# Kernel optimization log

Measured on AMD Instinct MI355X. Metric: run time of the kernel, lower is better.

The kernel has to match this reference:

```python
import jax, jax.numpy as jnp
import numpy as np

D_MODEL = 1024
NUM_HEADS = 16
MAX_LEN = 500
D_K = D_MODEL // NUM_HEADS


def setup_inputs() -> dict:
    key = jax.random.key(0)
    ks = jax.random.split(key, 10)
    B, L = 8, 500
    s = 1.0 / np.sqrt(D_MODEL)
    return {
        "query": jax.random.normal(ks[0], (B, L, D_MODEL), dtype=jnp.float32),
        "key": jax.random.normal(ks[1], (B, L, D_MODEL), dtype=jnp.float32),
        "value": jax.random.normal(ks[2], (B, L, D_MODEL), dtype=jnp.float32),
        "Wq": jax.random.normal(ks[3], (D_MODEL, D_MODEL), dtype=jnp.float32) * s,
        "bq": jnp.zeros((D_MODEL,), dtype=jnp.float32),
        "Wk": jax.random.normal(ks[4], (D_MODEL, D_MODEL), dtype=jnp.float32) * s,
        "bk": jnp.zeros((D_MODEL,), dtype=jnp.float32),
        "Wv": jax.random.normal(ks[5], (D_MODEL, D_MODEL), dtype=jnp.float32) * s,
        "bv": jnp.zeros((D_MODEL,), dtype=jnp.float32),
        "rel_emb": jax.random.normal(ks[6], (NUM_HEADS, 2 * MAX_LEN - 1), dtype=jnp.float32),
    }


def reference(query, key, value, Wq, bq, Wk, bk, Wv, bv, rel_emb):
    B, Lq, _ = query.shape
    Lk = key.shape[1]
    H, dk = NUM_HEADS, D_K
    # QKV projections -> [B, H, L, d]
    q = (query @ Wq + bq).reshape(B, Lq, H, dk).transpose(0, 2, 1, 3)
    k = (key @ Wk + bk).reshape(B, Lk, H, dk).transpose(0, 2, 1, 3)
    v = (value @ Wv + bv).reshape(B, Lk, H, dk).transpose(0, 2, 1, 3)
    scores = jnp.einsum('bhqd,bhkd->bhqk', q, k) / jnp.sqrt(jnp.float32(dk))
    # gathered relative-position bias: [H, Lq, Lk]
    rel_idx = jnp.arange(Lq)[:, None] - jnp.arange(Lk)[None, :] + MAX_LEN - 1
    bias = rel_emb[:, rel_idx]  # [H, Lq, Lk]
    scores = scores + bias[None]
    attn = jax.nn.softmax(scores, axis=-1)
    out = jnp.einsum('bhqk,bhkd->bhqd', attn, v)
    return out.transpose(0, 2, 1, 3).reshape(B, Lq, H * dk)
```

## Files before the change

### kernel.cpp

```cpp
#include <hip/hip_runtime.h>

typedef short bf16x8 __attribute__((ext_vector_type(8)));
typedef float f32x4 __attribute__((ext_vector_type(4)));
typedef unsigned uint4v __attribute__((ext_vector_type(4)));

#define B_    8
#define L_    500
#define LP    512
#define H_    16
#define DK    64
#define DM    1024
#define MP    4096
#define NT    8

static __device__ __forceinline__ unsigned short f2bf(float x) {
  unsigned u = __float_as_uint(x);
  u += 0x7fffu + ((u >> 16) & 1u);
  return (unsigned short)(u >> 16);
}

static __device__ __forceinline__ unsigned cvtpk(float lo, float hi) {
  unsigned r;
  asm("v_cvt_pk_bf16_f32 %0, %1, %2" : "=v"(r) : "v"(lo), "v"(hi));
  return r;
}

static __device__ __forceinline__ void gload16(const void* g, void* l) {
  __builtin_amdgcn_global_load_lds(
      (const __attribute__((address_space(1))) void*)g,
      (__attribute__((address_space(3))) void*)l, 16, 0, 0);
}

__global__ __launch_bounds__(256) void conv_x_kernel(
    const float* __restrict__ iq, const float* __restrict__ ik,
    const float* __restrict__ iv, unsigned short* __restrict__ X) {
  const int z = blockIdx.y;
  const float* src = (z == 0) ? iq : (z == 1) ? ik : iv;
  const size_t flat = (size_t)blockIdx.x * 256 + threadIdx.x;
  const size_t off = flat * 8;
  const int m = (int)(off >> 10);
  unsigned short o[8];
  if (m < 4000) {
    const float4 a = *(const float4*)(src + off);
    const float4 b = *(const float4*)(src + off + 4);
    o[0]=f2bf(a.x); o[1]=f2bf(a.y); o[2]=f2bf(a.z); o[3]=f2bf(a.w);
    o[4]=f2bf(b.x); o[5]=f2bf(b.y); o[6]=f2bf(b.z); o[7]=f2bf(b.w);
  } else {
#pragma unroll
    for (int i = 0; i < 8; ++i) o[i] = 0;
  }
  uint4 pk;
  pk.x = (unsigned)o[0] | ((unsigned)o[1] << 16);
  pk.y = (unsigned)o[2] | ((unsigned)o[3] << 16);
  pk.z = (unsigned)o[4] | ((unsigned)o[5] << 16);
  pk.w = (unsigned)o[6] | ((unsigned)o[7] << 16);
  *(uint4*)(X + (size_t)z * MP * DM + off) = pk;
}

__global__ __launch_bounds__(256) void conv_w_kernel(
    const float* __restrict__ wq, const float* __restrict__ wk,
    const float* __restrict__ wv, unsigned short* __restrict__ Wt) {
  const int z = blockIdx.y;
  const float* W = (z == 0) ? wq : (z == 1) ? wk : wv;
  const int k0 = (blockIdx.x >> 4) * 64;
  const int n0 = (blockIdx.x & 15) * 64;
  __shared__ float t[64][65];
  const int tid = threadIdx.x;
  const int row = tid >> 2;
  const int cb  = (tid & 3) * 16;
#pragma unroll
  for (int s = 0; s < 4; ++s) {
    const float4 v = *(const float4*)(W + (size_t)(k0 + row) * DM + n0 + cb + s * 4);
    t[row][cb + s * 4 + 0] = v.x; t[row][cb + s * 4 + 1] = v.y;
    t[row][cb + s * 4 + 2] = v.z; t[row][cb + s * 4 + 3] = v.w;
  }
  __syncthreads();
  const int nr = tid >> 2;
  const int kb = (tid & 3) * 16;
#pragma unroll
  for (int s = 0; s < 2; ++s) {
    unsigned short o[8];
#pragma unroll
    for (int e = 0; e < 8; ++e) o[e] = f2bf(t[kb + s * 8 + e][nr]);
    uint4 pk;
    pk.x = (unsigned)o[0] | ((unsigned)o[1] << 16);
    pk.y = (unsigned)o[2] | ((unsigned)o[3] << 16);
    pk.z = (unsigned)o[4] | ((unsigned)o[5] << 16);
    pk.w = (unsigned)o[6] | ((unsigned)o[7] << 16);
    *(uint4*)(Wt + (size_t)z * DM * DM + (size_t)(n0 + nr) * DM + k0 + kb + s * 8) = pk;
  }
}

__global__ __launch_bounds__(256) void gemm_qkv_kernel(
    const unsigned short* __restrict__ X, const unsigned short* __restrict__ Wt,
    const float* __restrict__ bq, const float* __restrict__ bk,
    const float* __restrict__ bv,
    unsigned short* __restrict__ qo, unsigned short* __restrict__ ko,
    unsigned short* __restrict__ vo) {
  const int z = blockIdx.y;
  const unsigned short* A  = X  + (size_t)z * MP * DM;
  const unsigned short* Bw = Wt + (size_t)z * DM * DM;
  const float* bias = (z == 0) ? bq : (z == 1) ? bk : bv;
  unsigned short* out = (z == 0) ? qo : (z == 1) ? ko : vo;

  const int bid = blockIdx.x;
  const int xg = bid & 7, y = bid >> 3;
  const int tm = xg + 8 * (y >> 3);
  const int tn = y & 7;
  const int tid = threadIdx.x;
  const int lane = tid & 63, wid = tid >> 6;
  const int wr = wid >> 1, wc = wid & 1;
  const int lg = lane >> 4, lr = lane & 15;

  __shared__ unsigned short sA[2][128 * 32];
  __shared__ unsigned short sB[2][128 * 32];

  const int c0 = tid, c1 = tid + 256;
  const int ar0 = c0 >> 2, ak0 = (c0 & 3) * 8;
  const int ar1 = c1 >> 2, ak1 = (c1 & 3) * 8;
  const unsigned short* Ab = A  + (size_t)tm * 128 * DM;
  const unsigned short* Bb = Bw + (size_t)tn * 128 * DM;

  f32x4 acc[4][4];
#pragma unroll
  for (int i = 0; i < 4; ++i)
#pragma unroll
    for (int j = 0; j < 4; ++j) acc[i][j] = (f32x4){0.f, 0.f, 0.f, 0.f};

  gload16(Ab + (size_t)ar0 * DM + ak0, &sA[0][c0 * 8]);
  gload16(Ab + (size_t)ar1 * DM + ak1, &sA[0][c1 * 8]);
  gload16(Bb + (size_t)ar0 * DM + ak0, &sB[0][c0 * 8]);
  gload16(Bb + (size_t)ar1 * DM + ak1, &sB[0][c1 * 8]);
  asm volatile("s_waitcnt vmcnt(0)" ::: "memory");
  __syncthreads();

  int cur = 0;
  for (int t = 0; t < 32; ++t) {
    if (t < 31) {
      const int kn = (t + 1) * 32;
      gload16(Ab + (size_t)ar0 * DM + kn + ak0, &sA[cur ^ 1][c0 * 8]);
      gload16(Ab + (size_t)ar1 * DM + kn + ak1, &sA[cur ^ 1][c1 * 8]);
      gload16(Bb + (size_t)ar0 * DM + kn + ak0, &sB[cur ^ 1][c0 * 8]);
      gload16(Bb + (size_t)ar1 * DM + kn + ak1, &sB[cur ^ 1][c1 * 8]);
    }
    bf16x8 af[4], bfr[4];
#pragma unroll
    for (int s = 0; s < 4; ++s) {
      af[s]  = *(const bf16x8*)&sA[cur][(wr * 64 + s * 16 + lr) * 32 + lg * 8];
      bfr[s] = *(const bf16x8*)&sB[cur][(wc * 64 + s * 16 + lr) * 32 + lg * 8];
    }
#pragma unroll
    for (int i = 0; i < 4; ++i)
#pragma unroll
      for (int j = 0; j < 4; ++j)
        acc[i][j] = __builtin_amdgcn_mfma_f32_16x16x32_bf16(af[i], bfr[j], acc[i][j], 0, 0, 0);
    asm volatile("s_waitcnt vmcnt(0)" ::: "memory");
    __syncthreads();
    cur ^= 1;
  }

  const int nbase = tn * 128 + wc * 64 + lr;
  float bias4[4];
#pragma unroll
  for (int ns = 0; ns < 4; ++ns) bias4[ns] = bias[nbase + ns * 16];

#pragma unroll
  for (int ms = 0; ms < 4; ++ms) {
#pragma unroll
    for (int r = 0; r < 4; ++r) {
      const int m = tm * 128 + wr * 64 + ms * 16 + lg * 4 + r;
      if (m < 4000) {
        const unsigned batch = (unsigned)m / 500u;
        const int lrow = m - (int)batch * 500;
#pragma unroll
        for (int ns = 0; ns < 4; ++ns) {
          const int n = nbase + ns * 16;
          const int hh = n >> 6, d = n & 63;
          out[(((size_t)batch * H_ + hh) * LP + lrow) * DK + d] =
              f2bf(acc[ms][ns][r] + bias4[ns]);
        }
      }
    }
  }
}

__global__ __launch_bounds__(256) void transpose_v_kernel(
    const unsigned short* __restrict__ v, unsigned short* __restrict__ vt) {
  const int bh = blockIdx.y;
  const int l0 = blockIdx.x * 64;
  __shared__ unsigned short t[64][72];
  const int tid = threadIdx.x;
  const int lrw = tid >> 2, dc = (tid & 3) * 16;
  const int gl = l0 + lrw;
  if (gl < L_) {
    *(uint4*)&t[lrw][dc]     = *(const uint4*)(v + ((size_t)bh * LP + gl) * DK + dc);
    *(uint4*)&t[lrw][dc + 8] = *(const uint4*)(v + ((size_t)bh * LP + gl) * DK + dc + 8);
  } else {
    const uint4 zz = {0u, 0u, 0u, 0u};
    *(uint4*)&t[lrw][dc]     = zz;
    *(uint4*)&t[lrw][dc + 8] = zz;
  }
  __syncthreads();
  const int dr = tid >> 2, lcb = (tid & 3) * 16;
#pragma unroll
  for (int s = 0; s < 2; ++s) {
    unsigned short e[8];
#pragma unroll
    for (int i = 0; i < 8; ++i) e[i] = t[lcb + s * 8 + i][dr];
    uint4 o;
    o.x = (unsigned)e[0] | ((unsigned)e[1] << 16);
    o.y = (unsigned)e[2] | ((unsigned)e[3] << 16);
    o.z = (unsigned)e[4] | ((unsigned)e[5] << 16);
    o.w = (unsigned)e[6] | ((unsigned)e[7] << 16);
    *(uint4*)(vt + ((size_t)bh * DK + dr) * LP + l0 + lcb + s * 8) = o;
  }
}

__global__ __launch_bounds__(256, 4) void attn_kernel(
    const unsigned short* __restrict__ q, const unsigned short* __restrict__ k,
    const unsigned short* __restrict__ vt, const float* __restrict__ rel,
    float* __restrict__ out) {
  const int id = blockIdx.x;
  const int bh = id & 127, qc = id >> 7;
  const int b = bh >> 4, h = bh & 15;
  const int tid = threadIdx.x;
  const int lane = tid & 63, wid = tid >> 6;
  const int lg = lane >> 4, lr = lane & 15;

  __shared__ unsigned short kt[2][2][64][32];
  __shared__ unsigned short vtt[2][2][64][32];
  __shared__ float relb[576];

  const float LOG2E = 1.44269504f;
  const float SC = 0.125f * LOG2E;
  const int rbase = qc * 64 - 12;
  for (int i = tid; i < 575; i += 256) {
    int idx = rbase + i;
    idx = idx < 0 ? 0 : (idx > 998 ? 998 : idx);
    relb[i] = rel[h * 999 + idx] * LOG2E;
  }

  const int qrow = qc * 64 + wid * 16 + lr;
  const unsigned short* qp = q + ((size_t)bh * LP + qrow) * DK + lg * 8;
  const bf16x8 qf0 = *(const bf16x8*)qp;
  const bf16x8 qf1 = *(const bf16x8*)(qp + 32);

  const int kj = tid >> 2, dc = (tid & 3) * 16;
  const unsigned short* kgp = k + ((size_t)bh * LP + kj) * DK + dc;
  unsigned short* kls = &kt[0][dc >> 5][kj][dc & 31];
  const int vd = tid >> 2, vkg = (tid & 3) * 16;
  const unsigned short* vgp = vt + ((size_t)bh * DK + vd) * LP + vkg;
  unsigned short* vls = &vtt[0][vkg >> 5][vd][vkg & 31];

  const int sig0 = 8 * (lr >> 2) + (lr & 3);
  const int qin = wid * 16 + lr;

  f32x4 o[4];
#pragma unroll
  for (int d = 0; d < 4; ++d) o[d] = (f32x4){0.f, 0.f, 0.f, 0.f};
  float mrun = -1e30f, lrun = 0.f;

  uint4 ka0 = *(const uint4*)(kgp);
  uint4 ka1 = *(const uint4*)(kgp + 8);
  uint4 va0 = *(const uint4*)(vgp);
  uint4 va1 = *(const uint4*)(vgp + 8);

  for (int t = 0; t < NT; ++t) {
    const int buf = t & 1;
    *(uint4*)(kls + buf * 4096)     = ka0;
    *(uint4*)(kls + buf * 4096 + 8) = ka1;
    *(uint4*)(vls + buf * 4096)     = va0;
    *(uint4*)(vls + buf * 4096 + 8) = va1;
    __syncthreads();

    if (t < NT - 1) {
      const size_t ko_ = (size_t)(t + 1) * 64 * DK;
      ka0 = *(const uint4*)(kgp + ko_);
      ka1 = *(const uint4*)(kgp + ko_ + 8);
      va0 = *(const uint4*)(vgp + (t + 1) * 64);
      va1 = *(const uint4*)(vgp + (t + 1) * 64 + 8);
    }

    f32x4 s[2][2];
#pragma unroll
    for (int kc = 0; kc < 2; ++kc)
#pragma unroll
      for (int hf = 0; hf < 2; ++hf) {
        const int sg = kc * 32 + hf * 4 + sig0;
        const bf16x8 a0 = *(const bf16x8*)&kt[buf][0][sg][lg * 8];
        const bf16x8 a1 = *(const bf16x8*)&kt[buf][1][sg][lg * 8];
        f32x4 ss = (f32x4){0.f, 0.f, 0.f, 0.f};
        ss = __builtin_amdgcn_mfma_f32_16x16x32_bf16(a0, qf0, ss, 0, 0, 0);
        ss = __builtin_amdgcn_mfma_f32_16x16x32_bf16(a1, qf1, ss, 0, 0, 0);
        s[kc][hf] = ss;
      }

    float sc[2][2][4];
#pragma unroll
    for (int kc = 0; kc < 2; ++kc)
#pragma unroll
      for (int hf = 0; hf < 2; ++hf) {
        const int bidx = qin - (t * 64 + kc * 32 + 8 * lg + 4 * hf) + 511;
#pragma unroll
        for (int r = 0; r < 4; ++r)
          sc[kc][hf][r] = s[kc][hf][r] * SC + relb[bidx - r];
      }
    if (t == NT - 1) {
#pragma unroll
      for (int hf = 0; hf < 2; ++hf)
#pragma unroll
        for (int r = 0; r < 4; ++r)
          if (8 * lg + 4 * hf + r >= 20) sc[1][hf][r] = -1e30f;
    }

    float m0 = fmaxf(fmaxf(sc[0][0][0], sc[0][0][1]), fmaxf(sc[0][0][2], sc[0][0][3]));
    float m1 = fmaxf(fmaxf(sc[0][1][0], sc[0][1][1]), fmaxf(sc[0][1][2], sc[0][1][3]));
    float m2 = fmaxf(fmaxf(sc[1][0][0], sc[1][0][1]), fmaxf(sc[1][0][2], sc[1][0][3]));
    float m3 = fmaxf(fmaxf(sc[1][1][0], sc[1][1][1]), fmaxf(sc[1][1][2], sc[1][1][3]));
    const float mloc = fmaxf(fmaxf(m0, m1), fmaxf(m2, m3));
    if (!__all(mloc - mrun <= 11.5f)) {
      float mx = fmaxf(mloc, mrun);
      mx = fmaxf(mx, __shfl_xor(mx, 16));
      mx = fmaxf(mx, __shfl_xor(mx, 32));
      const float alpha = exp2f(mrun - mx);
      mrun = mx;
      lrun *= alpha;
#pragma unroll
      for (int d = 0; d < 4; ++d) {
        o[d][0] *= alpha; o[d][1] *= alpha; o[d][2] *= alpha; o[d][3] *= alpha;
      }
    }

    float rs = 0.f;
    unsigned pw[2][4];
#pragma unroll
    for (int kc = 0; kc < 2; ++kc)
#pragma unroll
      for (int hf = 0; hf < 2; ++hf) {
        float p0 = exp2f(sc[kc][hf][0] - mrun);
        float p1 = exp2f(sc[kc][hf][1] - mrun);
        float p2 = exp2f(sc[kc][hf][2] - mrun);
        float p3 = exp2f(sc[kc][hf][3] - mrun);
        rs += (p0 + p1) + (p2 + p3);
        pw[kc][hf * 2 + 0] = cvtpk(p0, p1);
        pw[kc][hf * 2 + 1] = cvtpk(p2, p3);
      }
    rs += __shfl_xor(rs, 16);
    rs += __shfl_xor(rs, 32);
    lrun += rs;

#pragma unroll
    for (int kc = 0; kc < 2; ++kc) {
      union { uint4v u; bf16x8 v; } cv;
      cv.u = (uint4v){pw[kc][0], pw[kc][1], pw[kc][2], pw[kc][3]};
      const bf16x8 pf = cv.v;
#pragma unroll
      for (int db = 0; db < 4; ++db) {
        const bf16x8 vf = *(const bf16x8*)&vtt[buf][kc][db * 16 + lr][lg * 8];
        o[db] = __builtin_amdgcn_mfma_f32_16x16x32_bf16(vf, pf, o[db], 0, 0, 0);
      }
    }
  }

  if (qrow < L_) {
    const float inv = 1.0f / lrun;
    float* op = out + ((size_t)b * L_ + qrow) * DM + h * DK + lg * 4;
#pragma unroll
    for (int db = 0; db < 4; ++db) {
      float4 v;
      v.x = o[db][0] * inv; v.y = o[db][1] * inv;
      v.z = o[db][2] * inv; v.w = o[db][3] * inv;
      *(float4*)(op + db * 16) = v;
    }
  }
}

extern "C" void kernel_launch(void* const* d_in, const int* in_sizes, int n_in,
                              void* d_out, int out_size, void* d_ws, size_t ws_size,
                              hipStream_t stream) {
  const float* iq  = (const float*)d_in[0];
  const float* ik  = (const float*)d_in[1];
  const float* iv  = (const float*)d_in[2];
  const float* wq  = (const float*)d_in[3];
  const float* bq  = (const float*)d_in[4];
  const float* wk  = (const float*)d_in[5];
  const float* bk  = (const float*)d_in[6];
  const float* wv  = (const float*)d_in[7];
  const float* bv  = (const float*)d_in[8];
  const float* rel = (const float*)d_in[9];
  float* out = (float*)d_out;

  char* w = (char*)d_ws;
  unsigned short* X   = (unsigned short*)(w);
  unsigned short* Wt  = (unsigned short*)(w + 25165824);
  unsigned short* qb  = (unsigned short*)(w + 31457280);
  unsigned short* kb  = (unsigned short*)(w + 39845888);
  unsigned short* vb  = (unsigned short*)(w + 48234496);
  unsigned short* vtb = (unsigned short*)(w);

  conv_x_kernel<<<dim3(2048, 3), 256, 0, stream>>>(iq, ik, iv, X);
  conv_w_kernel<<<dim3(256, 3), 256, 0, stream>>>(wq, wk, wv, Wt);
  gemm_qkv_kernel<<<dim3(256, 3), 256, 0, stream>>>(X, Wt, bq, bk, bv, qb, kb, vb);
  transpose_v_kernel<<<dim3(8, 128), 256, 0, stream>>>(vb, vtb);
  attn_kernel<<<1024, 256, 0, stream>>>(qb, kb, vtb, rel, out);
}
```

Measured before the change: 90.91 us.

## Merge conversion kernels and triple-buffer QKV GEMM loads

Combines the activation and weight fp32-to-bf16 conversion kernels into one launch, dispatching on block index. The QKV GEMM moves from double to triple-buffered LDS staging, prefetching two tiles ahead with partial vmcnt waits and raw s_barrier instead of a full drain each iteration. This is meant to cut one launch and hide more global-load latency, at the cost of 50% more LDS per block, which could reduce occupancy. The transposed-V buffer also moves to its own workspace offset instead of aliasing X.

Measured after the change: 88.99 us. 1.02x faster.

```diff
diff --git a/kernel.cpp b/kernel.cpp
--- a/kernel.cpp
+++ b/kernel.cpp
@@ -31,41 +31,46 @@
       (__attribute__((address_space(3))) void*)l, 16, 0, 0);
 }
 
-__global__ __launch_bounds__(256) void conv_x_kernel(
+static __device__ __forceinline__ f32x4 MF(bf16x8 a, bf16x8 b, f32x4 c) {
+  return __builtin_amdgcn_mfma_f32_16x16x32_bf16(a, b, c, 0, 0, 0);
+}
+
+__global__ __launch_bounds__(256) void conv_kernel(
     const float* __restrict__ iq, const float* __restrict__ ik,
-    const float* __restrict__ iv, unsigned short* __restrict__ X) {
+    const float* __restrict__ iv,
+    const float* __restrict__ wq, const float* __restrict__ wk,
+    const float* __restrict__ wv,
+    unsigned short* __restrict__ X, unsigned short* __restrict__ Wt) {
   const int z = blockIdx.y;
-  const float* src = (z == 0) ? iq : (z == 1) ? ik : iv;
-  const size_t flat = (size_t)blockIdx.x * 256 + threadIdx.x;
-  const size_t off = flat * 8;
-  const int m = (int)(off >> 10);
-  unsigned short o[8];
-  if (m < 4000) {
-    const float4 a = *(const float4*)(src + off);
-    const float4 b = *(const float4*)(src + off + 4);
-    o[0]=f2bf(a.x); o[1]=f2bf(a.y); o[2]=f2bf(a.z); o[3]=f2bf(a.w);
-    o[4]=f2bf(b.x); o[5]=f2bf(b.y); o[6]=f2bf(b.z); o[7]=f2bf(b.w);
-  } else {
-#pragma unroll
-    for (int i = 0; i < 8; ++i) o[i] = 0;
-  }
-  uint4 pk;
-  pk.x = (unsigned)o[0] | ((unsigned)o[1] << 16);
-  pk.y = (unsigned)o[2] | ((unsigned)o[3] << 16);
-  pk.z = (unsigned)o[4] | ((unsigned)o[5] << 16);
-  pk.w = (unsigned)o[6] | ((unsigned)o[7] << 16);
-  *(uint4*)(X + (size_t)z * MP * DM + off) = pk;
-}
-
-__global__ __launch_bounds__(256) void conv_w_kernel(
-    const float* __restrict__ wq, const float* __restrict__ wk,
-    const float* __restrict__ wv, unsigned short* __restrict__ Wt) {
-  const int z = blockIdx.y;
+  const int bx = blockIdx.x;
+  const int tid = threadIdx.x;
+  if (bx < 2048) {
+    const float* src = (z == 0) ? iq : (z == 1) ? ik : iv;
+    const size_t off = ((size_t)bx * 256 + tid) * 8;
+    const int m = (int)(off >> 10);
+    unsigned short o[8];
+    if (m < 4000) {
+      const float4 a = *(const float4*)(src + off);
+      const float4 b = *(const float4*)(src + off + 4);
+      o[0]=f2bf(a.x); o[1]=f2bf(a.y); o[2]=f2bf(a.z); o[3]=f2bf(a.w);
+      o[4]=f2bf(b.x); o[5]=f2bf(b.y); o[6]=f2bf(b.z); o[7]=f2bf(b.w);
+    } else {
+#pragma unroll
+      for (int i = 0; i < 8; ++i) o[i] = 0;
+    }
+    uint4 pk;
+    pk.x = (unsigned)o[0] | ((unsigned)o[1] << 16);
+    pk.y = (unsigned)o[2] | ((unsigned)o[3] << 16);
+    pk.z = (unsigned)o[4] | ((unsigned)o[5] << 16);
+    pk.w = (unsigned)o[6] | ((unsigned)o[7] << 16);
+    *(uint4*)(X + (size_t)z * MP * DM + off) = pk;
+    return;
+  }
+  const int bw = bx - 2048;
   const float* W = (z == 0) ? wq : (z == 1) ? wk : wv;
-  const int k0 = (blockIdx.x >> 4) * 64;
-  const int n0 = (blockIdx.x & 15) * 64;
+  const int k0 = (bw >> 4) * 64;
+  const int n0 = (bw & 15) * 64;
   __shared__ float t[64][65];
-  const int tid = threadIdx.x;
   const int row = tid >> 2;
   const int cb  = (tid & 3) * 16;
 #pragma unroll
@@ -112,8 +117,8 @@
   const int wr = wid >> 1, wc = wid & 1;
   const int lg = lane >> 4, lr = lane & 15;
 
-  __shared__ unsigned short sA[2][128 * 32];
-  __shared__ unsigned short sB[2][128 * 32];
+  __shared__ __attribute__((aligned(16))) unsigned short sA[3][128 * 32];
+  __shared__ __attribute__((aligned(16))) unsigned short sB[3][128 * 32];
 
   const int c0 = tid, c1 = tid + 256;
   const int ar0 = c0 >> 2, ak0 = (c0 & 3) * 8;
@@ -121,42 +126,46 @@
   const unsigned short* Ab = A  + (size_t)tm * 128 * DM;
   const unsigned short* Bb = Bw + (size_t)tn * 128 * DM;
 
+  auto STAGE = [&](int t) {
+    const int buf = t % 3;
+    const int kn = t * 32;
+    gload16(Ab + (size_t)ar0 * DM + kn + ak0, &sA[buf][c0 * 8]);
+    gload16(Ab + (size_t)ar1 * DM + kn + ak1, &sA[buf][c1 * 8]);
+    gload16(Bb + (size_t)ar0 * DM + kn + ak0, &sB[buf][c0 * 8]);
+    gload16(Bb + (size_t)ar1 * DM + kn + ak1, &sB[buf][c1 * 8]);
+  };
+
   f32x4 acc[4][4];
 #pragma unroll
   for (int i = 0; i < 4; ++i)
 #pragma unroll
     for (int j = 0; j < 4; ++j) acc[i][j] = (f32x4){0.f, 0.f, 0.f, 0.f};
 
-  gload16(Ab + (size_t)ar0 * DM + ak0, &sA[0][c0 * 8]);
-  gload16(Ab + (size_t)ar1 * DM + ak1, &sA[0][c1 * 8]);
-  gload16(Bb + (size_t)ar0 * DM + ak0, &sB[0][c0 * 8]);
-  gload16(Bb + (size_t)ar1 * DM + ak1, &sB[0][c1 * 8]);
-  asm volatile("s_waitcnt vmcnt(0)" ::: "memory");
-  __syncthreads();
-
-  int cur = 0;
+  STAGE(0); STAGE(1);
+  asm volatile("s_waitcnt vmcnt(4)" ::: "memory");
+  __builtin_amdgcn_s_barrier();
+  __builtin_amdgcn_sched_barrier(0);
+
   for (int t = 0; t < 32; ++t) {
+    if (t < 30) STAGE(t + 2);
+    const int cb = t % 3;
+    bf16x8 af[4], bfr[4];
+#pragma unroll
+    for (int s = 0; s < 4; ++s) {
+      af[s]  = *(const bf16x8*)&sA[cb][(wr * 64 + s * 16 + lr) * 32 + lg * 8];
+      bfr[s] = *(const bf16x8*)&sB[cb][(wc * 64 + s * 16 + lr) * 32 + lg * 8];
+    }
+#pragma unroll
+    for (int i = 0; i < 4; ++i)
+#pragma unroll
+      for (int j = 0; j < 4; ++j)
+        acc[i][j] = MF(af[i], bfr[j], acc[i][j]);
     if (t < 31) {
-      const int kn = (t + 1) * 32;
-      gload16(Ab + (size_t)ar0 * DM + kn + ak0, &sA[cur ^ 1][c0 * 8]);
-      gload16(Ab + (size_t)ar1 * DM + kn + ak1, &sA[cur ^ 1][c1 * 8]);
-      gload16(Bb + (size_t)ar0 * DM + kn + ak0, &sB[cur ^ 1][c0 * 8]);
-      gload16(Bb + (size_t)ar1 * DM + kn + ak1, &sB[cur ^ 1][c1 * 8]);
-    }
-    bf16x8 af[4], bfr[4];
-#pragma unroll
-    for (int s = 0; s < 4; ++s) {
-      af[s]  = *(const bf16x8*)&sA[cur][(wr * 64 + s * 16 + lr) * 32 + lg * 8];
-      bfr[s] = *(const bf16x8*)&sB[cur][(wc * 64 + s * 16 + lr) * 32 + lg * 8];
-    }
-#pragma unroll
-    for (int i = 0; i < 4; ++i)
-#pragma unroll
-      for (int j = 0; j < 4; ++j)
-        acc[i][j] = __builtin_amdgcn_mfma_f32_16x16x32_bf16(af[i], bfr[j], acc[i][j], 0, 0, 0);
-    asm volatile("s_waitcnt vmcnt(0)" ::: "memory");
-    __syncthreads();
-    cur ^= 1;
+      if (t < 30) asm volatile("s_waitcnt vmcnt(4)" ::: "memory");
+      else        asm volatile("s_waitcnt vmcnt(0)" ::: "memory");
+      __builtin_amdgcn_s_barrier();
+      __builtin_amdgcn_sched_barrier(0);
+    }
   }
 
   const int nbase = tn * 128 + wc * 64 + lr;
@@ -396,10 +405,9 @@
   unsigned short* qb  = (unsigned short*)(w + 31457280);
   unsigned short* kb  = (unsigned short*)(w + 39845888);
   unsigned short* vb  = (unsigned short*)(w + 48234496);
-  unsigned short* vtb = (unsigned short*)(w);
-
-  conv_x_kernel<<<dim3(2048, 3), 256, 0, stream>>>(iq, ik, iv, X);
-  conv_w_kernel<<<dim3(256, 3), 256, 0, stream>>>(wq, wk, wv, Wt);
+  unsigned short* vtb = (unsigned short*)(w + 56623104);
+
+  conv_kernel<<<dim3(2304, 3), 256, 0, stream>>>(iq, ik, iv, wq, wk, wv, X, Wt);
   gemm_qkv_kernel<<<dim3(256, 3), 256, 0, stream>>>(X, Wt, bq, bk, bv, qb, kb, vb);
   transpose_v_kernel<<<dim3(8, 128), 256, 0, stream>>>(vb, vtb);
   attn_kernel<<<1024, 256, 0, stream>>>(qb, kb, vtb, rel, out);
```
